# Kernel optimization log

Hardware: AMD Instinct MI355X
Metric: run time of the kernel (lower is better)

## Reference

```python
import jax, jax.numpy as jnp
import numpy as np

N_SRC0, N_DST0 = 200000, 40000
N_SRC1, N_DST1 = 40000, 8000
E0, E1 = 1000000, 80000
D_IN, D_HID, D_OUT = 256, 512, 256


def setup_inputs() -> dict:
    key = jax.random.key(0)
    ks = jax.random.split(key, 10)
    return {
        "feat": jax.random.normal(ks[0], (N_SRC0, D_IN), dtype=jnp.float32),
        "Wself0": jax.random.normal(ks[1], (D_IN, D_HID), dtype=jnp.float32) * 0.05,
        "Wneigh0": jax.random.normal(ks[2], (D_IN, D_HID), dtype=jnp.float32) * 0.05,
        "b0": jnp.zeros((D_HID,), dtype=jnp.float32),
        "Wself1": jax.random.normal(ks[3], (D_HID, D_OUT), dtype=jnp.float32) * 0.05,
        "Wneigh1": jax.random.normal(ks[4], (D_HID, D_OUT), dtype=jnp.float32) * 0.05,
        "b1": jnp.zeros((D_OUT,), dtype=jnp.float32),
        "edge_src0": jax.random.randint(ks[5], (E0,), 0, N_SRC0, dtype=jnp.int32),
        "edge_dst0": jax.random.randint(ks[6], (E0,), 0, N_DST0, dtype=jnp.int32),
        "edge_src1": jax.random.randint(ks[7], (E1,), 0, N_SRC1, dtype=jnp.int32),
        "edge_dst1": jax.random.randint(ks[8], (E1,), 0, N_DST1, dtype=jnp.int32),
    }


def _mean_agg(h_src, src, dst, n_dst):
    # gather src features along edges, segment-mean over dst nodes
    msg_sum = jax.ops.segment_sum(h_src[src], dst, num_segments=n_dst)  # [n_dst, d]
    deg = jax.ops.segment_sum(jnp.ones(dst.shape, h_src.dtype), dst, num_segments=n_dst)
    return msg_sum / jnp.maximum(deg, 1.0)[:, None]


def _sage_layer(h, src, dst, n_dst, W_self, W_neigh, b):
    # DGL SAGEConv(mean): fc_self(h_dst) + fc_neigh(mean_neighbors) + bias
    h_dst = h[:n_dst]
    h_neigh = _mean_agg(h, src, dst, n_dst)
    return h_dst @ W_self + h_neigh @ W_neigh + b


def reference(feat, Wself0, Wneigh0, b0, Wself1, Wneigh1, b1,
              edge_src0, edge_dst0, edge_src1, edge_dst1):
    h = _sage_layer(feat, edge_src0, edge_dst0, N_DST0, Wself0, Wneigh0, b0)
    h = jax.nn.relu(h)  # ReLU between layers, not after last
    h = _sage_layer(h, edge_src1, edge_dst1, N_DST1, Wself1, Wneigh1, b1)
    return h
```

## Files before the change

### kernel.cpp

```cpp
#include <hip/hip_runtime.h>

#define DEV __device__ __forceinline__

typedef float f32x4 __attribute__((ext_vector_type(4)));
typedef short s16x4 __attribute__((ext_vector_type(4)));
typedef short s16x8 __attribute__((ext_vector_type(8)));

DEV float bf2f(short s) {
  unsigned u = ((unsigned)(unsigned short)s) << 16;
  return __builtin_bit_cast(float, u);
}
DEV short f2bf(float f) {
  unsigned u = __builtin_bit_cast(unsigned, f);
  u += 0x7FFFu + ((u >> 16) & 1u);
  return (short)(u >> 16);
}

DEV void gld_lds16(const void* g, void* l) {
  __builtin_amdgcn_global_load_lds(
      (const __attribute__((address_space(1))) void*)g,
      (__attribute__((address_space(3))) void*)l, 16, 0, 0);
}

__global__ void f32_to_bf16_k(const float* __restrict__ in, short* __restrict__ out, long n) {
  long i = ((long)blockIdx.x * blockDim.x + threadIdx.x) * 4;
  long stride = (long)gridDim.x * blockDim.x * 4;
  for (; i < n; i += stride) {
    f32x4 v = *(const f32x4*)(in + i);
    s16x4 o;
    o[0] = f2bf(v[0]); o[1] = f2bf(v[1]); o[2] = f2bf(v[2]); o[3] = f2bf(v[3]);
    *(s16x4*)(out + i) = o;
  }
}

__global__ void build_wt2_k(const float* __restrict__ Ws0, const float* __restrict__ Wn0,
                            short* __restrict__ W0T,
                            const float* __restrict__ Ws1, const float* __restrict__ Wn1,
                            short* __restrict__ W1T) {
  const int b = blockIdx.x, tid = threadIdx.x;
  if (b < 1024) {
    int idx = b * 256 + tid;
    if (idx < 512 * 512) {
      int n = idx >> 9, k = idx & 511;
      float v = (k < 256) ? Ws0[(size_t)k * 512 + n] : Wn0[(size_t)(k - 256) * 512 + n];
      W0T[idx] = f2bf(v);
    }
  } else {
    int idx = (b - 1024) * 256 + tid;
    if (idx < 256 * 1024) {
      int n = idx >> 10, k = idx & 1023;
      float v = (k < 512) ? Ws1[(size_t)k * 256 + n] : Wn1[(size_t)(k - 512) * 256 + n];
      W1T[idx] = f2bf(v);
    }
  }
}

__global__ void fillp2_k(const int* __restrict__ es0, const int* __restrict__ ed0, int E0,
                         int* __restrict__ cnt0, int* __restrict__ bk0,
                         const int* __restrict__ es1, const int* __restrict__ ed1, int E1,
                         int* __restrict__ cnt1, int* __restrict__ bk1) {
  const int b = blockIdx.x, tid = threadIdx.x;
  if (b < 936) {
    for (int e = b * 256 + tid; e < E0; e += 936 * 256) {
      int d = ed0[e];
      int p = atomicAdd(&cnt0[d], 1);
      if (p < 64) bk0[(d << 6) + p] = es0[e];
    }
  } else {
    for (int e = (b - 936) * 256 + tid; e < E1; e += 88 * 256) {
      int d = ed1[e];
      int p = atomicAdd(&cnt1[d], 1);
      if (p < 48) bk1[d * 48 + p] = es1[e];
    }
  }
}

__global__ void agg_f32_256(const float* __restrict__ X, const int* __restrict__ cntA,
                            const int* __restrict__ bucket, short* __restrict__ out,
                            int n_dst) {
  int gw = (blockIdx.x * blockDim.x + threadIdx.x) >> 6;
  if (gw >= n_dst) return;
  int lane = threadIdx.x & 63;
  int start = gw << 6, cnt = cntA[gw];
  float a[4] = {0, 0, 0, 0}, b[4] = {0, 0, 0, 0};
  int i = 0;
  for (; i + 2 <= cnt; i += 2) {
    int s0 = bucket[start + i], s1 = bucket[start + i + 1];
    f32x4 v0 = *(const f32x4*)(X + (size_t)s0 * 256 + lane * 4);
    f32x4 v1 = *(const f32x4*)(X + (size_t)s1 * 256 + lane * 4);
#pragma unroll
    for (int j = 0; j < 4; ++j) { a[j] += v0[j]; b[j] += v1[j]; }
  }
  if (i < cnt) {
    int s0 = bucket[start + i];
    f32x4 v0 = *(const f32x4*)(X + (size_t)s0 * 256 + lane * 4);
#pragma unroll
    for (int j = 0; j < 4; ++j) a[j] += v0[j];
  }
  float inv = 1.0f / (float)(cnt > 0 ? cnt : 1);
  s16x4 o;
#pragma unroll
  for (int j = 0; j < 4; ++j) o[j] = f2bf((a[j] + b[j]) * inv);
  *(s16x4*)(out + (size_t)gw * 256 + lane * 4) = o;
}

__global__ void agg_bf16_256(const short* __restrict__ X, const int* __restrict__ cntA,
                             const int* __restrict__ bucket, short* __restrict__ out,
                             int n_dst) {
  int gw = (blockIdx.x * blockDim.x + threadIdx.x) >> 6;
  if (gw >= n_dst) return;
  int lane = threadIdx.x & 63;
  int half = lane >> 5;
  int cl = lane & 31;
  int start = gw << 6, cnt = cntA[gw];
  float a[8] = {0, 0, 0, 0, 0, 0, 0, 0}, b[8] = {0, 0, 0, 0, 0, 0, 0, 0};
  int i = 0;
  for (; i + 4 <= cnt; i += 4) {
    int s0 = bucket[start + i + half];
    int s1 = bucket[start + i + 2 + half];
    s16x8 v0 = *(const s16x8*)(X + (size_t)s0 * 256 + cl * 8);
    s16x8 v1 = *(const s16x8*)(X + (size_t)s1 * 256 + cl * 8);
#pragma unroll
    for (int j = 0; j < 8; ++j) { a[j] += bf2f(v0[j]); b[j] += bf2f(v1[j]); }
  }
  for (; i < cnt; i += 2) {
    int idx = i + half;
    if (idx < cnt) {
      int s0 = bucket[start + idx];
      s16x8 v0 = *(const s16x8*)(X + (size_t)s0 * 256 + cl * 8);
#pragma unroll
      for (int j = 0; j < 8; ++j) a[j] += bf2f(v0[j]);
    }
  }
  float inv = 1.0f / (float)(cnt > 0 ? cnt : 1);
  float r[8];
#pragma unroll
  for (int j = 0; j < 8; ++j) {
    float s = a[j] + b[j];
    r[j] = s + __shfl(s, lane ^ 32);
  }
  if (half == 0) {
    s16x8 o;
#pragma unroll
    for (int j = 0; j < 8; ++j) o[j] = f2bf(r[j] * inv);
    *(s16x8*)(out + (size_t)gw * 256 + cl * 8) = o;
  }
}

__global__ void agg_bf16_512(const short* __restrict__ X, const int* __restrict__ cntA,
                             const int* __restrict__ bucket, short* __restrict__ out,
                             int n_dst) {
  int gw = (blockIdx.x * blockDim.x + threadIdx.x) >> 6;
  if (gw >= n_dst) return;
  int lane = threadIdx.x & 63;
  int start = gw * 48, cnt = cntA[gw];
  float a[8] = {0, 0, 0, 0, 0, 0, 0, 0}, b[8] = {0, 0, 0, 0, 0, 0, 0, 0};
  float c[8] = {0, 0, 0, 0, 0, 0, 0, 0}, d[8] = {0, 0, 0, 0, 0, 0, 0, 0};
  int i = 0;
  for (; i + 4 <= cnt; i += 4) {
    int s0 = bucket[start + i], s1 = bucket[start + i + 1];
    int s2 = bucket[start + i + 2], s3 = bucket[start + i + 3];
    s16x8 v0 = *(const s16x8*)(X + (size_t)s0 * 512 + lane * 8);
    s16x8 v1 = *(const s16x8*)(X + (size_t)s1 * 512 + lane * 8);
    s16x8 v2 = *(const s16x8*)(X + (size_t)s2 * 512 + lane * 8);
    s16x8 v3 = *(const s16x8*)(X + (size_t)s3 * 512 + lane * 8);
#pragma unroll
    for (int j = 0; j < 8; ++j) {
      a[j] += bf2f(v0[j]); b[j] += bf2f(v1[j]);
      c[j] += bf2f(v2[j]); d[j] += bf2f(v3[j]);
    }
  }
  for (; i < cnt; ++i) {
    int s0 = bucket[start + i];
    s16x8 v0 = *(const s16x8*)(X + (size_t)s0 * 512 + lane * 8);
#pragma unroll
    for (int j = 0; j < 8; ++j) a[j] += bf2f(v0[j]);
  }
  float inv = 1.0f / (float)(cnt > 0 ? cnt : 1);
  s16x8 o;
#pragma unroll
  for (int j = 0; j < 8; ++j) o[j] = f2bf(((a[j] + b[j]) + (c[j] + d[j])) * inv);
  *(s16x8*)(out + (size_t)gw * 512 + lane * 8) = o;
}

template <bool RELU_BF16>
__global__ __launch_bounds__(256, 2) void gemm_k(
    const short* __restrict__ Aleft, const short* __restrict__ Aright,
    const short* __restrict__ Bt, const float* __restrict__ bias,
    void* __restrict__ Cout, int M, int N, int K, int KH) {
  __shared__ short As[128 * 64];
  __shared__ short Bs[128 * 64];
  const int tid = threadIdx.x;
  const int w = tid >> 6, lane = tid & 63;
  const int m0 = blockIdx.y * 128, n0 = blockIdx.x * 128;
  const int wr = w >> 1, wc = w & 1;
  const int lr = lane & 15, lk = (lane >> 4) << 3;

  f32x4 acc[4][4] = {};

  const int nkt = K >> 6;
  const int ktH = KH >> 6;
  const size_t ldA = (size_t)KH * 2;
  const size_t ldB = (size_t)K * 2;

  for (int kt = 0; kt < nkt; ++kt) {
    const char* Abase = (const char*)((kt < ktH) ? Aleft : Aright);
    const int ktl = (kt < ktH) ? kt : kt - ktH;
#pragma unroll
    for (int j = 0; j < 4; ++j) {
      int o = ((w * 4 + j) << 10) + lane * 16;
      int row = o >> 7;
      int kb = o & 127;
      int kbs = kb ^ ((row & 7) << 4);
      int ar = m0 + row; if (ar > M - 1) ar = M - 1;
      gld_lds16(Abase + (size_t)ar * ldA + (size_t)(ktl * 128 + kbs),
                ((char*)As) + ((w * 4 + j) << 10));
      gld_lds16((const char*)Bt + (size_t)(n0 + row) * ldB + (size_t)(kt * 128 + kbs),
                ((char*)Bs) + ((w * 4 + j) << 10));
    }
    __syncthreads();
#pragma unroll
    for (int kk = 0; kk < 2; ++kk) {
      s16x8 af[4], bfr[4];
      const int kbyte = (kk * 32 + lk) * 2;
#pragma unroll
      for (int m = 0; m < 4; ++m) {
        int r = wr * 64 + m * 16 + lr;
        af[m] = *(const s16x8*)((const char*)As + (r << 7) + (kbyte ^ ((r & 7) << 4)));
      }
#pragma unroll
      for (int n = 0; n < 4; ++n) {
        int r = wc * 64 + n * 16 + lr;
        bfr[n] = *(const s16x8*)((const char*)Bs + (r << 7) + (kbyte ^ ((r & 7) << 4)));
      }
#pragma unroll
      for (int m = 0; m < 4; ++m)
#pragma unroll
        for (int n = 0; n < 4; ++n)
          acc[m][n] = __builtin_amdgcn_mfma_f32_16x16x32_bf16(af[m], bfr[n], acc[m][n], 0, 0, 0);
    }
    __syncthreads();
  }

  const int rq = (lane >> 4) * 4;
#pragma unroll
  for (int m = 0; m < 4; ++m) {
#pragma unroll
    for (int n = 0; n < 4; ++n) {
      const int col = n0 + wc * 64 + n * 16 + lr;
      const float bv = bias[col];
#pragma unroll
      for (int j = 0; j < 4; ++j) {
        const int row = m0 + wr * 64 + m * 16 + rq + j;
        if (row < M) {
          float v = acc[m][n][j] + bv;
          if (RELU_BF16) {
            v = v > 0.0f ? v : 0.0f;
            ((short*)Cout)[(size_t)row * N + col] = f2bf(v);
          } else {
            ((float*)Cout)[(size_t)row * N + col] = v;
          }
        }
      }
    }
  }
}

extern "C" void kernel_launch(void* const* d_in, const int* in_sizes, int n_in,
                              void* d_out, int out_size, void* d_ws, size_t ws_size,
                              hipStream_t stream) {
  const int NS0 = 200000, ND0 = 40000, ND1 = 8000;
  const int E0 = 1000000, E1 = 80000;
  const int DIN = 256, DH = 512, DOUT = 256;

  const float* feat = (const float*)d_in[0];
  const float* Wself0 = (const float*)d_in[1];
  const float* Wneigh0 = (const float*)d_in[2];
  const float* b0 = (const float*)d_in[3];
  const float* Wself1 = (const float*)d_in[4];
  const float* Wneigh1 = (const float*)d_in[5];
  const float* b1 = (const float*)d_in[6];
  const int* es0 = (const int*)d_in[7];
  const int* ed0 = (const int*)d_in[8];
  const int* es1 = (const int*)d_in[9];
  const int* ed1 = (const int*)d_in[10];

  char* w = (char*)d_ws;
  size_t pos = 0;
  auto take = [&](size_t b) -> char* {
    char* p = w + pos;
    pos += (b + 255) & ~(size_t)255;
    return p;
  };

  short* hne0 = (short*)take((size_t)ND0 * DIN * 2);
  short* h = (short*)take((size_t)ND0 * DH * 2);
  short* hne1 = (short*)take((size_t)ND1 * DH * 2);
  short* hdst0buf = (short*)take((size_t)ND0 * DIN * 2);
  short* W0T = (short*)take((size_t)DH * 2 * DIN * 2);
  short* W1T = (short*)take((size_t)DOUT * 2 * DH * 2);
  int* cnt0 = (int*)take((size_t)ND0 * 4);
  int* cnt1 = (int*)take((size_t)ND1 * 4);
  int* bucket0 = (int*)take((size_t)ND0 * 64 * 4);
  int* bucket1 = (int*)take((size_t)ND1 * 48 * 4);
  short* featbf = (short*)take((size_t)NS0 * DIN * 2);
  const bool use_bf = (ws_size >= pos);
  (void)in_sizes; (void)n_in; (void)out_size;

  hipMemsetAsync(cnt0, 0, (size_t)(ND0 + ND1) * 4, stream);

  const short* hdst0;
  if (use_bf) {
    f32_to_bf16_k<<<4096, 256, 0, stream>>>(feat, featbf, (long)NS0 * DIN);
    hdst0 = featbf;
  } else {
    f32_to_bf16_k<<<2048, 256, 0, stream>>>(feat, hdst0buf, (long)ND0 * DIN);
    hdst0 = hdst0buf;
  }

  build_wt2_k<<<2048, 256, 0, stream>>>(Wself0, Wneigh0, W0T, Wself1, Wneigh1, W1T);

  fillp2_k<<<1024, 256, 0, stream>>>(es0, ed0, E0, cnt0, bucket0,
                                     es1, ed1, E1, cnt1, bucket1);

  if (use_bf)
    agg_bf16_256<<<ND0 / 4, 256, 0, stream>>>(featbf, cnt0, bucket0, hne0, ND0);
  else
    agg_f32_256<<<ND0 / 4, 256, 0, stream>>>(feat, cnt0, bucket0, hne0, ND0);

  gemm_k<true><<<dim3(DH / 128, (ND0 + 127) / 128), 256, 0, stream>>>(
      hdst0, hne0, W0T, b0, h, ND0, DH, 2 * DIN, DIN);

  agg_bf16_512<<<ND1 / 4, 256, 0, stream>>>(h, cnt1, bucket1, hne1, ND1);

  gemm_k<false><<<dim3(DOUT / 128, (ND1 + 127) / 128), 256, 0, stream>>>(
      h, hne1, W1T, b1, (float*)d_out, ND1, DOUT, 2 * DH, DH);
}
```

Baseline: 296.2 us.

## Fold counter zeroing into weight kernel, widen conversion, use 64-row tiles for layer-1 GEMM

Drops the separate hipMemsetAsync by having extra blocks of the weight-transpose kernel zero the degree counters. The fp32-to-bf16 conversion now handles 8 elements per thread with a 16-byte store. The second-layer GEMM is templated on a 64-row M tile, which doubles its block count from 126 to 250 and improves occupancy on a small M. This trades a little per-block efficiency for better load balance and one fewer launch.

```diff
diff --git a/kernel.cpp b/kernel.cpp
--- a/kernel.cpp
+++ b/kernel.cpp
@@ -23,20 +23,22 @@
 }
 
 __global__ void f32_to_bf16_k(const float* __restrict__ in, short* __restrict__ out, long n) {
-  long i = ((long)blockIdx.x * blockDim.x + threadIdx.x) * 4;
-  long stride = (long)gridDim.x * blockDim.x * 4;
+  long i = ((long)blockIdx.x * blockDim.x + threadIdx.x) * 8;
+  long stride = (long)gridDim.x * blockDim.x * 8;
   for (; i < n; i += stride) {
-    f32x4 v = *(const f32x4*)(in + i);
-    s16x4 o;
-    o[0] = f2bf(v[0]); o[1] = f2bf(v[1]); o[2] = f2bf(v[2]); o[3] = f2bf(v[3]);
-    *(s16x4*)(out + i) = o;
+    f32x4 v0 = *(const f32x4*)(in + i);
+    f32x4 v1 = *(const f32x4*)(in + i + 4);
+    s16x8 o;
+    o[0] = f2bf(v0[0]); o[1] = f2bf(v0[1]); o[2] = f2bf(v0[2]); o[3] = f2bf(v0[3]);
+    o[4] = f2bf(v1[0]); o[5] = f2bf(v1[1]); o[6] = f2bf(v1[2]); o[7] = f2bf(v1[3]);
+    *(s16x8*)(out + i) = o;
   }
 }
 
 __global__ void build_wt2_k(const float* __restrict__ Ws0, const float* __restrict__ Wn0,
                             short* __restrict__ W0T,
                             const float* __restrict__ Ws1, const float* __restrict__ Wn1,
-                            short* __restrict__ W1T) {
+                            short* __restrict__ W1T, int* __restrict__ cntz) {
   const int b = blockIdx.x, tid = threadIdx.x;
   if (b < 1024) {
     int idx = b * 256 + tid;
@@ -45,13 +47,15 @@
       float v = (k < 256) ? Ws0[(size_t)k * 512 + n] : Wn0[(size_t)(k - 256) * 512 + n];
       W0T[idx] = f2bf(v);
     }
-  } else {
+  } else if (b < 2048) {
     int idx = (b - 1024) * 256 + tid;
     if (idx < 256 * 1024) {
       int n = idx >> 10, k = idx & 1023;
       float v = (k < 512) ? Ws1[(size_t)k * 256 + n] : Wn1[(size_t)(k - 512) * 256 + n];
       W1T[idx] = f2bf(v);
     }
+  } else {
+    for (int idx = (b - 2048) * 256 + tid; idx < 48000; idx += 188 * 256) cntz[idx] = 0;
   }
 }
 
@@ -183,20 +187,22 @@
   *(s16x8*)(out + (size_t)gw * 512 + lane * 8) = o;
 }
 
-template <bool RELU_BF16>
+template <int BM, bool RELU_BF16>
 __global__ __launch_bounds__(256, 2) void gemm_k(
     const short* __restrict__ Aleft, const short* __restrict__ Aright,
     const short* __restrict__ Bt, const float* __restrict__ bias,
     void* __restrict__ Cout, int M, int N, int K, int KH) {
-  __shared__ short As[128 * 64];
+  constexpr int MFR = BM / 32;
+  constexpr int PA = BM / 32;
+  __shared__ short As[BM * 64];
   __shared__ short Bs[128 * 64];
   const int tid = threadIdx.x;
   const int w = tid >> 6, lane = tid & 63;
-  const int m0 = blockIdx.y * 128, n0 = blockIdx.x * 128;
+  const int m0 = blockIdx.y * BM, n0 = blockIdx.x * 128;
   const int wr = w >> 1, wc = w & 1;
   const int lr = lane & 15, lk = (lane >> 4) << 3;
 
-  f32x4 acc[4][4] = {};
+  f32x4 acc[MFR][4] = {};
 
   const int nkt = K >> 6;
   const int ktH = KH >> 6;
@@ -207,25 +213,34 @@
     const char* Abase = (const char*)((kt < ktH) ? Aleft : Aright);
     const int ktl = (kt < ktH) ? kt : kt - ktH;
 #pragma unroll
-    for (int j = 0; j < 4; ++j) {
-      int o = ((w * 4 + j) << 10) + lane * 16;
+    for (int j = 0; j < PA; ++j) {
+      int c = w * PA + j;
+      int o = (c << 10) + lane * 16;
       int row = o >> 7;
       int kb = o & 127;
       int kbs = kb ^ ((row & 7) << 4);
       int ar = m0 + row; if (ar > M - 1) ar = M - 1;
       gld_lds16(Abase + (size_t)ar * ldA + (size_t)(ktl * 128 + kbs),
-                ((char*)As) + ((w * 4 + j) << 10));
+                ((char*)As) + (c << 10));
+    }
+#pragma unroll
+    for (int j = 0; j < 4; ++j) {
+      int c = w * 4 + j;
+      int o = (c << 10) + lane * 16;
+      int row = o >> 7;
+      int kb = o & 127;
+      int kbs = kb ^ ((row & 7) << 4);
       gld_lds16((const char*)Bt + (size_t)(n0 + row) * ldB + (size_t)(kt * 128 + kbs),
-                ((char*)Bs) + ((w * 4 + j) << 10));
+                ((char*)Bs) + (c << 10));
     }
     __syncthreads();
 #pragma unroll
     for (int kk = 0; kk < 2; ++kk) {
-      s16x8 af[4], bfr[4];
+      s16x8 af[MFR], bfr[4];
       const int kbyte = (kk * 32 + lk) * 2;
 #pragma unroll
-      for (int m = 0; m < 4; ++m) {
-        int r = wr * 64 + m * 16 + lr;
+      for (int m = 0; m < MFR; ++m) {
+        int r = wr * (BM / 2) + m * 16 + lr;
         af[m] = *(const s16x8*)((const char*)As + (r << 7) + (kbyte ^ ((r & 7) << 4)));
       }
 #pragma unroll
@@ -234,7 +249,7 @@
         bfr[n] = *(const s16x8*)((const char*)Bs + (r << 7) + (kbyte ^ ((r & 7) << 4)));
       }
 #pragma unroll
-      for (int m = 0; m < 4; ++m)
+      for (int m = 0; m < MFR; ++m)
 #pragma unroll
         for (int n = 0; n < 4; ++n)
           acc[m][n] = __builtin_amdgcn_mfma_f32_16x16x32_bf16(af[m], bfr[n], acc[m][n], 0, 0, 0);
@@ -244,14 +259,14 @@
 
   const int rq = (lane >> 4) * 4;
 #pragma unroll
-  for (int m = 0; m < 4; ++m) {
+  for (int m = 0; m < MFR; ++m) {
 #pragma unroll
     for (int n = 0; n < 4; ++n) {
       const int col = n0 + wc * 64 + n * 16 + lr;
       const float bv = bias[col];
 #pragma unroll
       for (int j = 0; j < 4; ++j) {
-        const int row = m0 + wr * 64 + m * 16 + rq + j;
+        const int row = m0 + wr * (BM / 2) + m * 16 + rq + j;
         if (row < M) {
           float v = acc[m][n][j] + bv;
           if (RELU_BF16) {
@@ -307,8 +322,6 @@
   const bool use_bf = (ws_size >= pos);
   (void)in_sizes; (void)n_in; (void)out_size;
 
-  hipMemsetAsync(cnt0, 0, (size_t)(ND0 + ND1) * 4, stream);
-
   const short* hdst0;
   if (use_bf) {
     f32_to_bf16_k<<<4096, 256, 0, stream>>>(feat, featbf, (long)NS0 * DIN);
@@ -318,7 +331,7 @@
     hdst0 = hdst0buf;
   }
 
-  build_wt2_k<<<2048, 256, 0, stream>>>(Wself0, Wneigh0, W0T, Wself1, Wneigh1, W1T);
+  build_wt2_k<<<2236, 256, 0, stream>>>(Wself0, Wneigh0, W0T, Wself1, Wneigh1, W1T, cnt0);
 
   fillp2_k<<<1024, 256, 0, stream>>>(es0, ed0, E0, cnt0, bucket0,
                                      es1, ed1, E1, cnt1, bucket1);
@@ -328,11 +341,11 @@
   else
     agg_f32_256<<<ND0 / 4, 256, 0, stream>>>(feat, cnt0, bucket0, hne0, ND0);
 
-  gemm_k<true><<<dim3(DH / 128, (ND0 + 127) / 128), 256, 0, stream>>>(
+  gemm_k<128, true><<<dim3(DH / 128, (ND0 + 127) / 128), 256, 0, stream>>>(
       hdst0, hne0, W0T, b0, h, ND0, DH, 2 * DIN, DIN);
 
   agg_bf16_512<<<ND1 / 4, 256, 0, stream>>>(h, cnt1, bucket1, hne1, ND1);
 
-  gemm_k<false><<<dim3(DOUT / 128, (ND1 + 127) / 128), 256, 0, stream>>>(
-      h, hne1, W1T, b1, (float*)d_out, ND1, DOUT, 2 * DH, DH);
-}
+  gemm_k<64, false><<<dim3(DOUT / 128, (ND1 + 63) / 64), 256, 0, stream>>>(
+      h, hne1, W1T, b1, d_out, ND1, DOUT, 2 * DH, DH);
+}
```

Measured after the change: 292.9 us. Within noise of the previous version (-1.1%).
